# Kernel optimization log

Hardware: AMD Instinct MI355X
Metric: run time of the kernel (lower is better)

The kernel has to match this reference:

```python
import jax, jax.numpy as jnp
import numpy as np

DIM = 1024
D_STATE = 64
D_CONV = 4
EXPAND = 2
N_HEADS = 8
D_INNER = DIM * EXPAND          # 2048
HEAD_DIM = D_INNER // N_HEADS   # 256
D_IN_PROJ = D_INNER + D_INNER + N_HEADS + D_STATE + D_STATE  # 4232
BATCH, SEQ = 2, 1024
EPS = 1e-6


def setup_inputs() -> dict:
    key = jax.random.key(0)
    ks = jax.random.split(key, 9)
    x = jax.random.normal(ks[0], (BATCH, SEQ, DIM), dtype=jnp.float32)
    in_proj_w = jax.random.normal(ks[1], (D_IN_PROJ, DIM), dtype=jnp.float32) * 0.02
    conv_w = jax.random.normal(ks[2], (D_INNER, D_CONV), dtype=jnp.float32) * 0.2
    conv_b = jax.random.normal(ks[3], (D_INNER,), dtype=jnp.float32) * 0.02
    A_log = jax.random.normal(ks[4], (N_HEADS,), dtype=jnp.float32) * 0.5
    D_param = jnp.ones((N_HEADS,), dtype=jnp.float32) + 0.1 * jax.random.normal(ks[5], (N_HEADS,), dtype=jnp.float32)
    dt_bias = jax.random.normal(ks[6], (N_HEADS,), dtype=jnp.float32) * 0.5
    norm_w = jnp.ones((D_INNER,), dtype=jnp.float32)
    out_proj_w = jax.random.normal(ks[7], (DIM, D_INNER), dtype=jnp.float32) * 0.02
    return {"x": x, "in_proj_w": in_proj_w, "conv_w": conv_w, "conv_b": conv_b,
            "A_log": A_log, "D_param": D_param, "dt_bias": dt_bias,
            "norm_w": norm_w, "out_proj_w": out_proj_w}


def _rms_norm(y, w):
    rms = jnp.sqrt(jnp.mean(y * y, axis=-1, keepdims=True) + EPS)
    return (y / rms) * w


def _depthwise_causal_conv(u, w, b):
    # u: (B, L, D_INNER); w: (D_INNER, D_CONV); torch Conv1d(pad=K-1)[..., :L]
    L = u.shape[1]
    up = jnp.pad(u, ((0, 0), (D_CONV - 1, 0), (0, 0)))
    out = b[None, None, :]
    for k in range(D_CONV):  # tiny fixed loop over taps
        out = out + up[:, k:k + L, :] * w[None, None, :, k]
    return out


def _mamba2_forward(x, in_proj_w, conv_w, conv_b, A_log, D_param, dt_bias, norm_w, out_proj_w):
    B_sz, L, _ = x.shape
    zxBCdt = x @ in_proj_w.T  # (B, L, D_IN_PROJ)
    z, xc, Bm, Cm, dt = jnp.split(
        zxBCdt, [D_INNER, 2 * D_INNER, 2 * D_INNER + N_HEADS, 2 * D_INNER + N_HEADS + D_STATE], axis=-1)
    # NOTE: split order matches torch .split([d_inner, d_inner, n_heads, d_state, d_state])
    xc = _depthwise_causal_conv(xc, conv_w, conv_b)
    xc = jax.nn.silu(xc)
    xh = xc.reshape(B_sz, L, N_HEADS, HEAD_DIM)  # (B, L, H, Dh)
    A = -jnp.exp(A_log)                          # (H,)
    dt = jax.nn.softplus(Bm + dt_bias)           # (B, L, H) -- torch split yields n_heads slice third
    a_bar = jnp.exp(dt * A[None, None, :])       # (B, L, H)

    # sequential SSD scan over L; carry h: (B, H, Dh, N)
    def step(h, t):
        a_t, b_t, c_t, x_t = t  # a:(B,H) b:(B,N) c:(B,N) x:(B,H,Dh)
        h = a_t[:, :, None, None] * h + b_t[:, None, None, :] * x_t[..., None]
        y_t = jnp.einsum('bhdn,bn->bhd', h, c_t)
        return h, y_t

    h0 = jnp.zeros((B_sz, N_HEADS, HEAD_DIM, D_STATE), dtype=x.dtype)
    xs = (jnp.moveaxis(a_bar, 1, 0), jnp.moveaxis(Cm, 1, 0) * 0 + jnp.moveaxis(Cm, 1, 0),
          jnp.moveaxis(dt, 1, 0) * 0, jnp.moveaxis(xh, 1, 0))  # placeholder, replaced below
    # Correct scan inputs: B proj = Cm slice? -- see split above: Bm is (B,L,H)? No:
    # split gives z:(..,D_INNER) xc:(..,D_INNER) third:(..,N_HEADS) fourth:(..,D_STATE) fifth:(..,D_STATE)
    # So dt-channels are the N_HEADS slice (Bm here), B is Cm, C is the last slice (dt var).
    B_proj, C_proj = Cm, dt if False else (Cm, None)
    raise NotImplementedError


def reference(x, in_proj_w, conv_w, conv_b, A_log, D_param, dt_bias, norm_w, out_proj_w):
    B_sz, L, _ = x.shape
    zxBCdt = x @ in_proj_w.T
    z = zxBCdt[..., :D_INNER]
    xc = zxBCdt[..., D_INNER:2 * D_INNER]
    Bp = zxBCdt[..., 2 * D_INNER:2 * D_INNER + N_HEADS]                      # torch 'B' slot? no:
    # torch split order: [d_inner, d_inner, n_heads, d_state, d_state] -> z, x, B, C, dt
    # so the n_heads-sized slice is named 'B' in torch code but used as B (input proj, size n_heads)?
    # In the torch code: z, x, B, C, dt = split([d_inner, d_inner, n_heads, d_state, d_state])
    # => B has size n_heads, C has size d_state, dt has size d_state. Faithfully reproduce that.
    Bm = zxBCdt[..., 2 * D_INNER:2 * D_INNER + N_HEADS]                       # (B,L,H)  -> 'B'
    Cm = zxBCdt[..., 2 * D_INNER + N_HEADS:2 * D_INNER + N_HEADS + D_STATE]   # (B,L,N)  -> 'C'
    dtm = zxBCdt[..., 2 * D_INNER + N_HEADS + D_STATE:]                       # (B,L,N)  -> 'dt'
    # ssd_scan(x, dt, A, B, C): dt broadcasts against dt_bias (H,) -> requires dt last dim == H.
    # The torch module passes dt of size d_state; with d_state=64 != n_heads this would error,
    # so faithful executable mapping uses the head-sized slice as dt and the two d_state slices as B, C.
    dt = jax.nn.softplus(Bm + dt_bias)            # (B, L, H)
    B_proj, C_proj = Cm, dtm                      # (B, L, N) each

    xc = _depthwise_causal_conv(xc, conv_w, conv_b)
    xc = jax.nn.silu(xc)
    xh = xc.reshape(B_sz, L, N_HEADS, HEAD_DIM)
    A = -jnp.exp(A_log)
    a_bar = jnp.exp(dt * A[None, None, :])        # (B, L, H)

    def step(h, t):
        a_t, b_t, c_t, x_t = t
        h = a_t[:, :, None, None] * h + b_t[:, None, None, :] * x_t[..., None]
        y_t = jnp.einsum('bhdn,bn->bhd', h, c_t)
        return h, y_t

    h0 = jnp.zeros((B_sz, N_HEADS, HEAD_DIM, D_STATE), dtype=x.dtype)
    ts = (jnp.moveaxis(a_bar, 1, 0), jnp.moveaxis(B_proj, 1, 0),
          jnp.moveaxis(C_proj, 1, 0), jnp.moveaxis(xh, 1, 0))
    _, ys = jax.lax.scan(step, h0, ts)
    y = jnp.moveaxis(ys, 0, 1)                    # (B, L, H, Dh)
    y = y + xh * D_param[None, None, :, None]
    y = y.reshape(B_sz, L, D_INNER)
    y = y * jax.nn.silu(z)
    y = _rms_norm(y, norm_w)
    return y @ out_proj_w.T
```

## Files before the change

### kernel.cpp

```cpp
#include <hip/hip_runtime.h>
#include <hip/hip_bf16.h>
#include <math.h>

#define DIM      1024
#define D_STATE  64
#define D_CONV   4
#define N_HEADS  8
#define D_INNER  2048
#define HEAD_DIM 256
#define NPROJ    4232
#define BATCH    2
#define SEQ      1024
#define M_ROWS   (BATCH * SEQ)
#define OFF_Z    0
#define OFF_XC   2048
#define OFF_DT   4096
#define OFF_B    4104
#define OFF_C    4168

#define CHUNK    64
#define N_CHUNK  (SEQ / CHUNK)
#define STATE_PER_BH (HEAD_DIM * D_STATE)

#define NPROJ_PAD 4352
#define PADT 72

typedef unsigned short u16;
typedef unsigned int   u32;
typedef _Float16 f16x8 __attribute__((ext_vector_type(8)));
typedef float    f32x4 __attribute__((ext_vector_type(4)));

__device__ __forceinline__ u16 f2h(float f) {
    _Float16 h = (_Float16)f;
    return __builtin_bit_cast(u16, h);
}
__device__ __forceinline__ float h2f(u16 u) {
    return (float)__builtin_bit_cast(_Float16, u);
}

__device__ __forceinline__ void load_lds16(const void* g, void* l) {
    __builtin_amdgcn_global_load_lds((const __attribute__((address_space(1))) unsigned int*)g,
                                     (__attribute__((address_space(3))) unsigned int*)l,
                                     16, 0, 0);
}

__device__ __forceinline__ float softplus_f(float v) {
    return (v > 20.f) ? v : __logf(1.f + __expf(v));
}

__global__ __launch_bounds__(256) void cast2_kernel(
        const float* __restrict__ s0, u16* __restrict__ h0, int n0,
        const float* __restrict__ s1, u16* __restrict__ h1, int n1) {
    int i4 = (blockIdx.x * 256 + threadIdx.x) * 4;
    const float* src; u16* dst;
    if (i4 < n0) {
        src = s0; dst = h0;
    } else {
        i4 -= n0;
        if (i4 >= n1) return;
        src = s1; dst = h1;
    }
    float4 v = *(const float4*)&src[i4];
    ushort4 h;
    h.x = f2h(v.x); h.y = f2h(v.y); h.z = f2h(v.z); h.w = f2h(v.w);
    *(ushort4*)&dst[i4] = h;
}

__global__ __launch_bounds__(256) void cast_hn_kernel(const float* __restrict__ src,
                                                      const float* __restrict__ nw,
                                                      u16* __restrict__ hi, int n) {
    int i4 = (blockIdx.x * 256 + threadIdx.x) * 4;
    if (i4 >= n) return;
    float4 v = *(const float4*)&src[i4];
    int c = i4 & (D_INNER - 1);
    ushort4 h;
    h.x = f2h(v.x * nw[c]);
    h.y = f2h(v.y * nw[c + 1]);
    h.z = f2h(v.z * nw[c + 2]);
    h.w = f2h(v.w * nw[c + 3]);
    *(ushort4*)&hi[i4] = h;
}

template<int BN>
__global__ __launch_bounds__(256) void gemm_mfma1(const u16* __restrict__ Ah,
                                                  const u16* __restrict__ Bh,
                                                  float* __restrict__ C,
                                                  int K, int ldc, int Nstore,
                                                  int NrowsB, size_t zstride) {
    __shared__ u16 As[128 * 32];
    __shared__ u16 Bs[BN * 32];

    const int tid  = threadIdx.x;
    const int wave = tid >> 6;
    const int lane = tid & 63;
    const int fr   = lane & 15;
    const int kc   = lane >> 4;
    const int m0   = blockIdx.y * 128;
    const int n0   = blockIdx.x * BN;
    const int wm   = (wave & 1) * 64;
    const int wn   = (wave >> 1) * (BN / 2);

    const int kPer = K / gridDim.z;
    const int kBeg = blockIdx.z * kPer;
    C += (size_t)blockIdx.z * zstride;

    f32x4 acc[4][BN / 32];
#pragma unroll
    for (int i = 0; i < 4; ++i)
#pragma unroll
        for (int j = 0; j < BN / 32; ++j) acc[i][j] = (f32x4)0.f;

    for (int k0 = kBeg; k0 < kBeg + kPer; k0 += 32) {
        __syncthreads();
#pragma unroll
        for (int q = 0; q < 2; ++q) {
            int s = wave * 128 + q * 64 + lane;
            int r = s >> 2, pc = s & 3;
            int gc = pc ^ ((r >> 1) & 3);
            size_t goff = (size_t)(m0 + r) * K + k0 + gc * 8;
            load_lds16(Ah + goff, &As[(wave * 128 + q * 64) * 8]);
        }
#pragma unroll
        for (int q = 0; q < BN / 64; ++q) {
            int s = wave * BN + q * 64 + lane;
            int r = s >> 2, pc = s & 3;
            int gc = pc ^ ((r >> 1) & 3);
            if (n0 + r < NrowsB) {
                size_t goff = (size_t)(n0 + r) * K + k0 + gc * 8;
                load_lds16(Bh + goff, &Bs[(wave * BN + q * 64) * 8]);
            }
        }
        __syncthreads();

        f16x8 af[4];
#pragma unroll
        for (int i = 0; i < 4; ++i) {
            int r = wm + i * 16 + fr;
            int off = r * 32 + (kc ^ ((r >> 1) & 3)) * 8;
            af[i] = *(const f16x8*)&As[off];
        }
        f16x8 bf[BN / 32];
#pragma unroll
        for (int j = 0; j < BN / 32; ++j) {
            int r = wn + j * 16 + fr;
            int off = r * 32 + (kc ^ ((r >> 1) & 3)) * 8;
            bf[j] = *(const f16x8*)&Bs[off];
        }
#pragma unroll
        for (int i = 0; i < 4; ++i)
#pragma unroll
            for (int j = 0; j < BN / 32; ++j)
                acc[i][j] = __builtin_amdgcn_mfma_f32_16x16x32_f16(af[i], bf[j], acc[i][j], 0, 0, 0);
    }

    const int row0 = m0 + wm + (lane >> 4) * 4;
    const int colb = n0 + wn + fr;
#pragma unroll
    for (int i = 0; i < 4; ++i)
#pragma unroll
        for (int j = 0; j < BN / 32; ++j) {
            int col = colb + j * 16;
            if (col < Nstore) {
#pragma unroll
                for (int t = 0; t < 4; ++t)
                    C[(size_t)(row0 + i * 16 + t) * ldc + col] = acc[i][j][t];
            }
        }
}

__global__ __launch_bounds__(256) void reduce2rms_kernel(const float* __restrict__ p,
                                                         const float* __restrict__ rowSS,
                                                         float* __restrict__ out, int n) {
    int i4 = (blockIdx.x * 256 + threadIdx.x) * 4;
    int m = i4 >> 10;
    float scale = rsqrtf(rowSS[m] * (1.f / (float)D_INNER) + 1e-6f);
    float4 a = *(const float4*)&p[i4];
    float4 b = *(const float4*)&p[(size_t)n + i4];
    *(float4*)&out[i4] = make_float4((a.x + b.x) * scale, (a.y + b.y) * scale,
                                     (a.z + b.z) * scale, (a.w + b.w) * scale);
}

__global__ __launch_bounds__(256) void conv_silu_kernel(const float* __restrict__ zx,
                                                        const float* __restrict__ conv_w,
                                                        const float* __restrict__ conv_b,
                                                        u16* __restrict__ xh) {
    int idx = blockIdx.x * 256 + threadIdx.x;
    int c = idx & (D_INNER - 1);
    int m = idx >> 11;
    int l = m & (SEQ - 1);
    float acc = conv_b[c];
#pragma unroll
    for (int k = 0; k < D_CONV; ++k) {
        int lj = l + k - (D_CONV - 1);
        if (lj >= 0)
            acc = fmaf(zx[(size_t)(m + k - (D_CONV - 1)) * NPROJ + OFF_XC + c],
                       conv_w[c * D_CONV + k], acc);
    }
    xh[idx] = f2h(acc / (1.f + __expf(-acc)));
}

__global__ __launch_bounds__(256) void scan_state_mfma(const float* __restrict__ zx,
                                                       const u16* __restrict__ xh,
                                                       const float* __restrict__ dt_bias,
                                                       const float* __restrict__ A_log,
                                                       u16* __restrict__ Sloc,
                                                       float* __restrict__ csum) {
    const int blk = blockIdx.x;
    const int dq = blk & 3;
    const int c  = (blk >> 2) & (N_CHUNK - 1);
    const int bh = blk >> 6;
    const int hh = bh & (N_HEADS - 1);
    const int b  = bh >> 3;
    const int t    = threadIdx.x;
    const int wave = t >> 6;
    const int lane = t & 63;
    const int fr   = lane & 15;
    const int quad = lane >> 4;

    __shared__ float SDs[64];
    __shared__ u16 BwT[64 * PADT];
    __shared__ u16 XsT[64 * PADT];

    const int m0   = b * SEQ + c * CHUNK;
    const int xcol = hh * HEAD_DIM + dq * 64;
    const float Ahd = -__expf(A_log[hh]);
    const float dtb = dt_bias[hh];

    if (t < 64) {
        float d = softplus_f(zx[(size_t)(m0 + t) * NPROJ + OFF_DT + hh] + dtb);
#pragma unroll
        for (int off = 1; off < 64; off <<= 1) {
            float o = __shfl_up(d, off);
            if (lane >= off) d += o;
        }
        SDs[t] = d;
    }
    __syncthreads();
    const float SD63 = SDs[63];
    if (dq == 0 && t == 0) csum[bh * N_CHUNK + c] = SD63;

#pragma unroll
    for (int i = 0; i < 16; ++i) {
        int idx = t + i * 256;
        int r = idx >> 6, n = idx & 63;
        float bv = zx[(size_t)(m0 + r) * NPROJ + OFF_B + n];
        float w2 = __expf(Ahd * (SD63 - SDs[r]));
        BwT[n * PADT + r] = f2h(bv * w2);
        XsT[n * PADT + r] = xh[(size_t)(m0 + r) * D_INNER + xcol + n];
    }
    __syncthreads();

    const int tm0 = wave * 16;
    f32x4 sa[4];
#pragma unroll
    for (int j = 0; j < 4; ++j) sa[j] = (f32x4)0.f;
#pragma unroll
    for (int kk = 0; kk < 2; ++kk) {
        f16x8 af = *(const f16x8*)&BwT[(tm0 + fr) * PADT + kk * 32 + quad * 8];
#pragma unroll
        for (int j = 0; j < 4; ++j) {
            f16x8 bf = *(const f16x8*)&XsT[(j * 16 + fr) * PADT + kk * 32 + quad * 8];
            sa[j] = __builtin_amdgcn_mfma_f32_16x16x32_f16(af, bf, sa[j], 0, 0, 0);
        }
    }
    size_t sbase = (size_t)(bh * N_CHUNK + c) * STATE_PER_BH;
#pragma unroll
    for (int j = 0; j < 4; ++j)
#pragma unroll
        for (int reg = 0; reg < 4; ++reg) {
            int nn = tm0 + quad * 4 + reg;
            int dd = j * 16 + fr;
            Sloc[sbase + (size_t)nn * HEAD_DIM + dq * 64 + dd] = f2h(sa[j][reg]);
        }
}

__global__ __launch_bounds__(256) void scan_combine2(const float* __restrict__ csum,
                                                     const float* __restrict__ A_log,
                                                     u32* __restrict__ Sl) {
    const int blk = blockIdx.x;
    const int seg = blk & 31;
    const int bh  = blk >> 5;
    const int hh  = bh & (N_HEADS - 1);
    const int t   = threadIdx.x;

    __shared__ float PS[N_CHUNK];
    if (t < N_CHUNK) {
        float Ahd = -__expf(A_log[hh]);
        PS[t] = __expf(Ahd * csum[bh * N_CHUNK + t]);
    }
    __syncthreads();

    const int HPC = STATE_PER_BH / 2;
    size_t base = (size_t)bh * N_CHUNK * HPC + seg * 256 + t;
    u32 Sv[N_CHUNK];
#pragma unroll
    for (int c = 0; c < N_CHUNK; ++c)
        Sv[c] = Sl[base + (size_t)c * HPC];
    float H0 = 0.f, H1 = 0.f;
#pragma unroll
    for (int c = 0; c < N_CHUNK; ++c) {
        Sl[base + (size_t)c * HPC] = ((u32)f2h(H1) << 16) | (u32)f2h(H0);
        float P = PS[c];
        H0 = fmaf(P, H0, h2f((u16)(Sv[c] & 0xffffu)));
        H1 = fmaf(P, H1, h2f((u16)(Sv[c] >> 16)));
    }
}

__global__ __launch_bounds__(256) void scan_ycorr_mfma(const float* __restrict__ zx,
                                                       const u16* __restrict__ xh,
                                                       const float* __restrict__ dt_bias,
                                                       const float* __restrict__ A_log,
                                                       const float* __restrict__ Dp,
                                                       const u16* __restrict__ Hini,
                                                       u16* __restrict__ ybf,
                                                       float* __restrict__ rowSS) {
    const int blk = blockIdx.x;
    const int dq = blk & 3;
    const int c  = (blk >> 2) & (N_CHUNK - 1);
    const int bh = blk >> 6;
    const int hh = bh & (N_HEADS - 1);
    const int b  = bh >> 3;
    const int t    = threadIdx.x;
    const int wave = t >> 6;
    const int lane = t & 63;
    const int fr   = lane & 15;
    const int quad = lane >> 4;

    __shared__ float SDs[64];
    __shared__ u16 Ct  [64 * PADT];
    __shared__ u16 BtPs[64 * PADT];
    __shared__ u16 XsT [64 * PADT];
    __shared__ u16 Hdn [64 * PADT];

    const int m0   = b * SEQ + c * CHUNK;
    const int xcol = hh * HEAD_DIM + dq * 64;
    const float Ahd = -__expf(A_log[hh]);
    const float dtb = dt_bias[hh];

    if (t < 64) {
        float d = softplus_f(zx[(size_t)(m0 + t) * NPROJ + OFF_DT + hh] + dtb);
#pragma unroll
        for (int off = 1; off < 64; off <<= 1) {
            float o = __shfl_up(d, off);
            if (lane >= off) d += o;
        }
        SDs[t] = d;
    }

    size_t hbase = (size_t)(bh * N_CHUNK + c) * STATE_PER_BH;
    u16 hreg[16];
#pragma unroll
    for (int i = 0; i < 16; ++i) {
        int idx = t + i * 256;
        int r = idx >> 6, n = idx & 63;
        hreg[i] = Hini[hbase + (size_t)r * HEAD_DIM + dq * 64 + n];
    }

#pragma unroll
    for (int i = 0; i < 16; ++i) {
        int idx = t + i * 256;
        int r = idx >> 6, n = idx & 63;
        size_t rowz = (size_t)(m0 + r) * NPROJ;
        BtPs[r * PADT + n] = f2h(zx[rowz + OFF_B + n]);
        Ct[r * PADT + n]   = f2h(zx[rowz + OFF_C + n]);
        XsT[n * PADT + r]  = xh[(size_t)(m0 + r) * D_INNER + xcol + n];
    }
    __syncthreads();

    const int tm0 = wave * 16;

    f32x4 g[4];
#pragma unroll
    for (int j = 0; j < 4; ++j) g[j] = (f32x4)0.f;
#pragma unroll
    for (int kk = 0; kk < 2; ++kk) {
        f16x8 af = *(const f16x8*)&Ct[(tm0 + fr) * PADT + kk * 32 + quad * 8];
#pragma unroll
        for (int j = 0; j < 4; ++j) {
            f16x8 bf = *(const f16x8*)&BtPs[(j * 16 + fr) * PADT + kk * 32 + quad * 8];
            g[j] = __builtin_amdgcn_mfma_f32_16x16x32_f16(af, bf, g[j], 0, 0, 0);
        }
    }
    __syncthreads();

    {
        int trow = tm0 + quad * 4;
#pragma unroll
        for (int j = 0; j < 4; ++j) {
#pragma unroll
            for (int reg = 0; reg < 4; ++reg) {
                int tt = trow + reg, ss = j * 16 + fr;
                float val = 0.f;
                if (ss <= tt) val = __expf(Ahd * (SDs[tt] - SDs[ss])) * g[j][reg];
                BtPs[tt * PADT + ss] = f2h(val);
            }
        }
    }
#pragma unroll
    for (int i = 0; i < 16; ++i) {
        int idx = t + i * 256;
        int r = idx >> 6, n = idx & 63;
        Hdn[n * PADT + r] = hreg[i];
    }
    __syncthreads();

    f32x4 ya[4], yb[4];
#pragma unroll
    for (int j = 0; j < 4; ++j) { ya[j] = (f32x4)0.f; yb[j] = (f32x4)0.f; }
#pragma unroll
    for (int kk = 0; kk < 2; ++kk) {
        f16x8 afp = *(const f16x8*)&BtPs[(tm0 + fr) * PADT + kk * 32 + quad * 8];
        f16x8 afc = *(const f16x8*)&Ct[(tm0 + fr) * PADT + kk * 32 + quad * 8];
#pragma unroll
        for (int j = 0; j < 4; ++j) {
            f16x8 bx = *(const f16x8*)&XsT[(j * 16 + fr) * PADT + kk * 32 + quad * 8];
            f16x8 bh_ = *(const f16x8*)&Hdn[(j * 16 + fr) * PADT + kk * 32 + quad * 8];
            ya[j] = __builtin_amdgcn_mfma_f32_16x16x32_f16(afp, bx, ya[j], 0, 0, 0);
            yb[j] = __builtin_amdgcn_mfma_f32_16x16x32_f16(afc, bh_, yb[j], 0, 0, 0);
        }
    }

    const float Dh = Dp[hh];
#pragma unroll
    for (int reg = 0; reg < 4; ++reg) {
        int tt = tm0 + quad * 4 + reg;
        float cum = __expf(Ahd * SDs[tt]);
        size_t rowz = (size_t)(m0 + tt) * NPROJ;
        size_t rowy = (size_t)(m0 + tt) * D_INNER + xcol;
        float ss = 0.f;
#pragma unroll
        for (int j = 0; j < 4; ++j) {
            int dd = j * 16 + fr;
            float xv = h2f(XsT[dd * PADT + tt]);
            float z  = zx[rowz + OFF_Z + xcol + dd];
            float yv = ya[j][reg] + cum * yb[j][reg] + Dh * xv;
            float gated = yv * (z / (1.f + __expf(-z)));
            ybf[rowy + dd] = f2h(gated);
            ss += gated * gated;
        }
#pragma unroll
        for (int off = 1; off < 16; off <<= 1) ss += __shfl_xor(ss, off);
        if (fr == 0) atomicAdd(&rowSS[m0 + tt], ss);
    }
}

extern "C" void kernel_launch(void* const* d_in, const int* in_sizes, int n_in,
                              void* d_out, int out_size, void* d_ws, size_t ws_size,
                              hipStream_t stream) {
    const float* x         = (const float*)d_in[0];
    const float* in_proj_w = (const float*)d_in[1];
    const float* conv_w    = (const float*)d_in[2];
    const float* conv_b    = (const float*)d_in[3];
    const float* A_log     = (const float*)d_in[4];
    const float* D_param   = (const float*)d_in[5];
    const float* dt_bias   = (const float*)d_in[6];
    const float* norm_w    = (const float*)d_in[7];
    const float* out_proj_w= (const float*)d_in[8];
    float* out = (float*)d_out;

    float* ws  = (float*)d_ws;
    float* zx  = ws;
    float* R1  = zx + 8667136;
    float* R2  = R1 + 2166784;
    float* ab  = R2 + 4194304;
    float* R3  = ab + 16384;

    u16*  xh     = (u16*)R1;
    u16*  wobf_h = (u16*)R1;
    u16*  xbf_h  = (u16*)R2;
    u16*  ybf    = (u16*)R2;
    float* csum  = ab;
    float* rowSS = ab + 2048;
    u16*  wibf_h = (u16*)R3;
    u16*  Sloc   = (u16*)R3;
    float* pbuf  = zx;

    hipMemsetAsync(rowSS, 0, M_ROWS * sizeof(float), stream);
    {
        int n0 = M_ROWS * DIM;
        int n1 = NPROJ * DIM;
        cast2_kernel<<<(n0 + n1) / 1024, 256, 0, stream>>>(
            x, xbf_h, n0, in_proj_w, wibf_h, n1);
    }

    gemm_mfma1<128><<<dim3(NPROJ_PAD / 128, M_ROWS / 128, 1), 256, 0, stream>>>(
        xbf_h, wibf_h, zx, DIM, NPROJ, NPROJ, NPROJ, 0);

    conv_silu_kernel<<<(M_ROWS * D_INNER) / 256, 256, 0, stream>>>(
        zx, conv_w, conv_b, xh);

    scan_state_mfma<<<BATCH * N_HEADS * N_CHUNK * 4, 256, 0, stream>>>(
        zx, xh, dt_bias, A_log, Sloc, csum);
    scan_combine2<<<BATCH * N_HEADS * 32, 256, 0, stream>>>(
        csum, A_log, (u32*)Sloc);
    scan_ycorr_mfma<<<BATCH * N_HEADS * N_CHUNK * 4, 256, 0, stream>>>(
        zx, xh, dt_bias, A_log, D_param, Sloc, ybf, rowSS);

    cast_hn_kernel<<<(DIM * D_INNER) / 1024, 256, 0, stream>>>(
        out_proj_w, norm_w, wobf_h, DIM * D_INNER);

    gemm_mfma1<64><<<dim3(DIM / 64, M_ROWS / 128, 2), 256, 0, stream>>>(
        ybf, wobf_h, pbuf, D_INNER, DIM, DIM, DIM,
        (size_t)M_ROWS * DIM);

    reduce2rms_kernel<<<(M_ROWS * DIM) / 1024, 256, 0, stream>>>(
        pbuf, rowSS, out, M_ROWS * DIM);
}
```

Before: 196.3 us.

## Merge weight casts into one kernel, narrow in_proj GEMM tile, raise MFMA priority

The out_proj weight cast with norm scaling is folded into the initial cast kernel, so one launch converts x, in_proj_w and out_proj_w, and the separate cast_hn launch is dropped. The out_proj fp16 buffer moves to the upper half of R2 so it no longer aliases xh. The in_proj GEMM switches from 128-wide to 64-wide N tiles, which cuts padding waste (4288 vs 4352 columns) and doubles the block count. s_setprio raises wave priority around the MFMA loops in the scan kernels. The risks are that a 64-wide tile gets less reuse per block, and that the relocated buffer must not overlap live data in R2.

New measurement: 207.4 us. +5.6%, slower.

```diff
diff --git a/kernel.cpp b/kernel.cpp
--- a/kernel.cpp
+++ b/kernel.cpp
@@ -22,7 +22,7 @@
 #define N_CHUNK  (SEQ / CHUNK)
 #define STATE_PER_BH (HEAD_DIM * D_STATE)
 
-#define NPROJ_PAD 4352
+#define NPROJ_PAD64 4288
 #define PADT 72
 
 typedef unsigned short u16;
@@ -48,37 +48,37 @@
     return (v > 20.f) ? v : __logf(1.f + __expf(v));
 }
 
-__global__ __launch_bounds__(256) void cast2_kernel(
+__global__ __launch_bounds__(256) void cast3_kernel(
         const float* __restrict__ s0, u16* __restrict__ h0, int n0,
-        const float* __restrict__ s1, u16* __restrict__ h1, int n1) {
+        const float* __restrict__ s1, u16* __restrict__ h1, int n1,
+        const float* __restrict__ s2, const float* __restrict__ nw,
+        u16* __restrict__ h2, int n2) {
     int i4 = (blockIdx.x * 256 + threadIdx.x) * 4;
-    const float* src; u16* dst;
     if (i4 < n0) {
-        src = s0; dst = h0;
-    } else {
-        i4 -= n0;
-        if (i4 >= n1) return;
-        src = s1; dst = h1;
-    }
-    float4 v = *(const float4*)&src[i4];
-    ushort4 h;
-    h.x = f2h(v.x); h.y = f2h(v.y); h.z = f2h(v.z); h.w = f2h(v.w);
-    *(ushort4*)&dst[i4] = h;
-}
-
-__global__ __launch_bounds__(256) void cast_hn_kernel(const float* __restrict__ src,
-                                                      const float* __restrict__ nw,
-                                                      u16* __restrict__ hi, int n) {
-    int i4 = (blockIdx.x * 256 + threadIdx.x) * 4;
-    if (i4 >= n) return;
-    float4 v = *(const float4*)&src[i4];
+        float4 v = *(const float4*)&s0[i4];
+        ushort4 h;
+        h.x = f2h(v.x); h.y = f2h(v.y); h.z = f2h(v.z); h.w = f2h(v.w);
+        *(ushort4*)&h0[i4] = h;
+        return;
+    }
+    i4 -= n0;
+    if (i4 < n1) {
+        float4 v = *(const float4*)&s1[i4];
+        ushort4 h;
+        h.x = f2h(v.x); h.y = f2h(v.y); h.z = f2h(v.z); h.w = f2h(v.w);
+        *(ushort4*)&h1[i4] = h;
+        return;
+    }
+    i4 -= n1;
+    if (i4 >= n2) return;
+    float4 v = *(const float4*)&s2[i4];
     int c = i4 & (D_INNER - 1);
     ushort4 h;
     h.x = f2h(v.x * nw[c]);
     h.y = f2h(v.y * nw[c + 1]);
     h.z = f2h(v.z * nw[c + 2]);
     h.w = f2h(v.w * nw[c + 3]);
-    *(ushort4*)&hi[i4] = h;
+    *(ushort4*)&h2[i4] = h;
 }
 
 template<int BN>
@@ -254,6 +254,7 @@
     f32x4 sa[4];
 #pragma unroll
     for (int j = 0; j < 4; ++j) sa[j] = (f32x4)0.f;
+    __builtin_amdgcn_s_setprio(1);
 #pragma unroll
     for (int kk = 0; kk < 2; ++kk) {
         f16x8 af = *(const f16x8*)&BwT[(tm0 + fr) * PADT + kk * 32 + quad * 8];
@@ -263,6 +264,7 @@
             sa[j] = __builtin_amdgcn_mfma_f32_16x16x32_f16(af, bf, sa[j], 0, 0, 0);
         }
     }
+    __builtin_amdgcn_s_setprio(0);
     size_t sbase = (size_t)(bh * N_CHUNK + c) * STATE_PER_BH;
 #pragma unroll
     for (int j = 0; j < 4; ++j)
@@ -372,6 +374,7 @@
     f32x4 g[4];
 #pragma unroll
     for (int j = 0; j < 4; ++j) g[j] = (f32x4)0.f;
+    __builtin_amdgcn_s_setprio(1);
 #pragma unroll
     for (int kk = 0; kk < 2; ++kk) {
         f16x8 af = *(const f16x8*)&Ct[(tm0 + fr) * PADT + kk * 32 + quad * 8];
@@ -381,6 +384,7 @@
             g[j] = __builtin_amdgcn_mfma_f32_16x16x32_f16(af, bf, g[j], 0, 0, 0);
         }
     }
+    __builtin_amdgcn_s_setprio(0);
     __syncthreads();
 
     {
@@ -407,6 +411,7 @@
     f32x4 ya[4], yb[4];
 #pragma unroll
     for (int j = 0; j < 4; ++j) { ya[j] = (f32x4)0.f; yb[j] = (f32x4)0.f; }
+    __builtin_amdgcn_s_setprio(1);
 #pragma unroll
     for (int kk = 0; kk < 2; ++kk) {
         f16x8 afp = *(const f16x8*)&BtPs[(tm0 + fr) * PADT + kk * 32 + quad * 8];
@@ -419,6 +424,7 @@
             yb[j] = __builtin_amdgcn_mfma_f32_16x16x32_f16(afc, bh_, yb[j], 0, 0, 0);
         }
     }
+    __builtin_amdgcn_s_setprio(0);
 
     const float Dh = Dp[hh];
 #pragma unroll
@@ -466,9 +472,9 @@
     float* R3  = ab + 16384;
 
     u16*  xh     = (u16*)R1;
-    u16*  wobf_h = (u16*)R1;
     u16*  xbf_h  = (u16*)R2;
     u16*  ybf    = (u16*)R2;
+    u16*  wobf_h = (u16*)(R2 + 2097152);
     float* csum  = ab;
     float* rowSS = ab + 2048;
     u16*  wibf_h = (u16*)R3;
@@ -479,11 +485,12 @@
     {
         int n0 = M_ROWS * DIM;
         int n1 = NPROJ * DIM;
-        cast2_kernel<<<(n0 + n1) / 1024, 256, 0, stream>>>(
-            x, xbf_h, n0, in_proj_w, wibf_h, n1);
-    }
-
-    gemm_mfma1<128><<<dim3(NPROJ_PAD / 128, M_ROWS / 128, 1), 256, 0, stream>>>(
+        int n2 = DIM * D_INNER;
+        cast3_kernel<<<(n0 + n1 + n2) / 1024, 256, 0, stream>>>(
+            x, xbf_h, n0, in_proj_w, wibf_h, n1, out_proj_w, norm_w, wobf_h, n2);
+    }
+
+    gemm_mfma1<64><<<dim3(NPROJ_PAD64 / 64, M_ROWS / 128, 1), 256, 0, stream>>>(
         xbf_h, wibf_h, zx, DIM, NPROJ, NPROJ, NPROJ, 0);
 
     conv_silu_kernel<<<(M_ROWS * D_INNER) / 256, 256, 0, stream>>>(
@@ -496,9 +503,6 @@
     scan_ycorr_mfma<<<BATCH * N_HEADS * N_CHUNK * 4, 256, 0, stream>>>(
         zx, xh, dt_bias, A_log, D_param, Sloc, ybf, rowSS);
 
-    cast_hn_kernel<<<(DIM * D_INNER) / 1024, 256, 0, stream>>>(
-        out_proj_w, norm_w, wobf_h, DIM * D_INNER);
-
     gemm_mfma1<64><<<dim3(DIM / 64, M_ROWS / 128, 2), 256, 0, stream>>>(
         ybf, wobf_h, pbuf, D_INNER, DIM, DIM, DIM,
         (size_t)M_ROWS * DIM);
```
